# Kernel optimization log

Hardware: AMD Instinct MI355X
Metric: run time of the kernel (lower is better)

Reference implementation:

```python
import jax, jax.numpy as jnp
import numpy as np

B, S, D, H = 4, 2048, 1024, 16
W = D // H  # head width = 64


def setup_inputs() -> dict:
    key = jax.random.key(0)
    ks = jax.random.split(key, 7)
    sc = 0.02
    return {
        "x": jax.random.normal(ks[0], (B, S, D), dtype=jnp.float32),
        "mask": jnp.ones((B, S), dtype=jnp.int32),
        "Wq": jax.random.normal(ks[1], (D, D), dtype=jnp.float32) * sc,
        "bq": jax.random.normal(ks[2], (D,), dtype=jnp.float32) * sc,
        "Wk": jax.random.normal(ks[3], (D, D), dtype=jnp.float32) * sc,
        "bk": jax.random.normal(ks[4], (D,), dtype=jnp.float32) * sc,
        "Wv": jax.random.normal(ks[5], (D, D), dtype=jnp.float32) * sc,
        "bv": jax.random.normal(ks[6], (D,), dtype=jnp.float32) * sc,
    }


def reference(x, mask, Wq, bq, Wk, bk, Wv, bv):
    # Linear projections (torch Linear: y = x @ W.T + b)
    q = x @ Wq.T + bq  # (B,S,D)
    k = x @ Wk.T + bk
    v = x @ Wv.T + bv
    # split D -> (H, W) and move heads forward: (B,H,S,W)
    def split(t):
        return t.reshape(B, S, H, W).transpose(0, 2, 1, 3)
    q, k, v = split(q), split(k), split(v)
    scale = 1.0 / np.sqrt(W).astype(np.float32)
    scores = jnp.einsum("bhsw,bhtw->bhst", q, k) * scale  # (B,H,S,S)
    m = mask[:, None, None, :].astype(scores.dtype)  # (B,1,1,S)
    scores = scores - 10000.0 * (1.0 - m)
    probs = jax.nn.softmax(scores, axis=-1)  # dropout p=0.0 -> identity
    h = jnp.einsum("bhst,bhtw->bhsw", probs, v)  # (B,H,S,W)
    h = h.transpose(0, 2, 1, 3).reshape(B, S, D)  # merge heads
    return h
```

## Files before the change

kernel.cpp:

```cpp
#include <hip/hip_runtime.h>
#include <hip/hip_bf16.h>


#define NB 4
#define NS 2048
#define ND 1024
#define NH 16
#define NW 64

typedef __bf16 bf16;
typedef __bf16 bf16x2 __attribute__((ext_vector_type(2)));
typedef __bf16 bf16x4 __attribute__((ext_vector_type(4)));
typedef __bf16 bf16x8 __attribute__((ext_vector_type(8)));
typedef float f32x4 __attribute__((ext_vector_type(4)));
typedef float f32x16 __attribute__((ext_vector_type(16)));
typedef unsigned u32x4 __attribute__((ext_vector_type(4)));

__device__ __forceinline__ void gld_lds16(const void* g, void* l) {
  __builtin_amdgcn_global_load_lds(
      (const __attribute__((address_space(1))) void*)g,
      (__attribute__((address_space(3))) void*)l, 16, 0, 0);
}

__device__ __forceinline__ unsigned pack2(float lo, float hi) {
  bf16x2 t;
  t[0] = (bf16)lo;
  t[1] = (bf16)hi;
  return __builtin_bit_cast(unsigned, t);
}

__global__ void cast_f32_bf16(const float* __restrict__ src,
                              bf16* __restrict__ dst, int n) {
  int i = (blockIdx.x * blockDim.x + threadIdx.x) * 8;
  int stride = gridDim.x * blockDim.x * 8;
  for (; i < n; i += stride) {
    float4 a = *reinterpret_cast<const float4*>(src + i);
    float4 b = *reinterpret_cast<const float4*>(src + i + 4);
    bf16x8 o;
    o[0] = (bf16)a.x; o[1] = (bf16)a.y; o[2] = (bf16)a.z; o[3] = (bf16)a.w;
    o[4] = (bf16)b.x; o[5] = (bf16)b.y; o[6] = (bf16)b.z; o[7] = (bf16)b.w;
    *reinterpret_cast<bf16x8*>(dst + i) = o;
  }
}

__global__ void cast_weights(const float* __restrict__ a,
                             const float* __restrict__ b,
                             const float* __restrict__ c,
                             bf16* __restrict__ dst) {
  const int n = ND * ND;
  const int which = blockIdx.y;
  const float* src = (which == 0) ? a : ((which == 1) ? b : c);
  bf16* d = dst + (size_t)which * n;
  int i = (blockIdx.x * blockDim.x + threadIdx.x) * 8;
  float4 u = *reinterpret_cast<const float4*>(src + i);
  float4 v = *reinterpret_cast<const float4*>(src + i + 4);
  bf16x8 o;
  o[0] = (bf16)u.x; o[1] = (bf16)u.y; o[2] = (bf16)u.z; o[3] = (bf16)u.w;
  o[4] = (bf16)v.x; o[5] = (bf16)v.y; o[6] = (bf16)v.z; o[7] = (bf16)v.w;
  *reinterpret_cast<bf16x8*>(d + i) = o;
}

__global__ void mask_to_bf16(const int* __restrict__ mask,
                             bf16* __restrict__ mb, int n) {
  int i = blockIdx.x * blockDim.x + threadIdx.x;
  if (i < n) mb[i] = (bf16)(mask[i] ? 1.0f : 0.0f);
}

__global__ __launch_bounds__(256) void proj_kernel(
    const bf16* __restrict__ xb,
    const bf16* __restrict__ wq,
    const bf16* __restrict__ wk,
    const bf16* __restrict__ wv,
    const float* __restrict__ bq,
    const float* __restrict__ bk,
    const float* __restrict__ bv,
    const int* __restrict__ mask,
    bf16* __restrict__ qh,
    bf16* __restrict__ kh,
    bf16* __restrict__ vt) {
  const int mode = blockIdx.z;
  const bf16* wmat = (mode == 0) ? wq : ((mode == 1) ? wk : wv);
  const float* bias = (mode == 0) ? bq : ((mode == 1) ? bk : bv);

  __shared__ bf16 a_lds[128][64];
  __shared__ bf16 b_lds[128][64];

  const int tid = threadIdx.x;
  const int wave = tid >> 6;
  const int lane = tid & 63;
  const int wr = wave >> 1, wc = wave & 1;
  const int m0 = blockIdx.x * 128;
  const int n0 = blockIdx.y * 128;

  f32x4 acc[4][4] = {};

  const int srow = tid >> 3;
  const int scol = (tid & 7) * 8;
  const int sw_scol = scol ^ ((srow & 7) << 3);
  const int xr = (lane & 7) << 3;
  const int lr = lane & 15;
  const int kq = (lane >> 4) * 8;

  for (int k0 = 0; k0 < 1024; k0 += 64) {
#pragma unroll
    for (int c = 0; c < 4; ++c) {
      int row = srow + c * 32;
      gld_lds16(xb + (size_t)(m0 + row) * 1024 + k0 + sw_scol, &a_lds[row][scol]);
      gld_lds16(wmat + (size_t)(n0 + row) * 1024 + k0 + sw_scol, &b_lds[row][scol]);
    }
    __syncthreads();
#pragma unroll
    for (int kk = 0; kk < 64; kk += 32) {
      bf16x8 af[4], bfr[4];
      const int col = (kk + kq) ^ xr;
#pragma unroll
      for (int mf = 0; mf < 4; ++mf)
        af[mf] = *reinterpret_cast<const bf16x8*>(&a_lds[wr * 64 + mf * 16 + lr][col]);
#pragma unroll
      for (int nf = 0; nf < 4; ++nf)
        bfr[nf] = *reinterpret_cast<const bf16x8*>(&b_lds[wc * 64 + nf * 16 + lr][col]);
#pragma unroll
      for (int mf = 0; mf < 4; ++mf)
#pragma unroll
        for (int nf = 0; nf < 4; ++nf)
          acc[mf][nf] = __builtin_amdgcn_mfma_f32_16x16x32_bf16(af[mf], bfr[nf], acc[mf][nf], 0, 0, 0);
    }
    __syncthreads();
  }

  if (mode == 2) {
    float msk[4][4];
#pragma unroll
    for (int mf = 0; mf < 4; ++mf) {
      const int i0 = m0 + wr * 64 + mf * 16 + (lane >> 4) * 4;
      const int b = i0 >> 11, s = i0 & 2047;
      const int4 mm = *reinterpret_cast<const int4*>(mask + b * NS + s);
      msk[mf][0] = mm.x ? 1.f : 0.f;
      msk[mf][1] = mm.y ? 1.f : 0.f;
      msk[mf][2] = mm.z ? 1.f : 0.f;
      msk[mf][3] = mm.w ? 1.f : 0.f;
    }
#pragma unroll
    for (int nf = 0; nf < 4; ++nf) {
      const int j = n0 + wc * 64 + nf * 16 + lr;
      const float bj = bias[j];
      const int h = j >> 6, w = j & 63;
#pragma unroll
      for (int mf = 0; mf < 4; ++mf) {
        const int i0 = m0 + wr * 64 + mf * 16 + (lane >> 4) * 4;
        const int b = i0 >> 11, s = i0 & 2047;
        bf16x4 pk;
#pragma unroll
        for (int r = 0; r < 4; ++r)
          pk[r] = (bf16)((acc[mf][nf][r] + bj) * msk[mf][r]);
        *reinterpret_cast<bf16x4*>(&vt[(((size_t)(b * NH + h)) * NW + w) * NS + s]) = pk;
      }
    }
  } else {
    bf16* dst = (mode == 0) ? qh : kh;
#pragma unroll
    for (int nf = 0; nf < 4; ++nf) {
      const int j = n0 + wc * 64 + nf * 16 + lr;
      const float bj = bias[j];
      const int h = j >> 6, w = j & 63;
#pragma unroll
      for (int mf = 0; mf < 4; ++mf) {
        const int i0 = m0 + wr * 64 + mf * 16 + (lane >> 4) * 4;
        const int b = i0 >> 11, s = i0 & 2047;
#pragma unroll
        for (int r = 0; r < 4; ++r)
          dst[(((size_t)(b * NH + h)) * NS + s + r) * NW + w] = (bf16)(acc[mf][nf][r] + bj);
      }
    }
  }
}

__global__ __launch_bounds__(256, 4) void attn_kernel(
    const bf16* __restrict__ qh,
    const bf16* __restrict__ kh,
    const bf16* __restrict__ vt,
    const bf16* __restrict__ mb16,
    float* __restrict__ out) {
  __shared__ bf16 k_lds[2][64][64];
  __shared__ bf16 v_lds[2][64][64];

  const int tid = threadIdx.x;
  const int wave = tid >> 6;
  const int lane = tid & 63;
  const int lq = lane & 31;
  const int hi = lane >> 5;
  const int xr = (lq & 7) << 3;
  const int bh = blockIdx.y;
  const int b = bh >> 4;
  const int q0 = blockIdx.x * 128;
  const size_t headoff = (size_t)bh * NS * NW;

  bf16x8 qf[4];
  {
    const bf16* qp = qh + headoff + (size_t)(q0 + wave * 32 + lq) * NW + hi * 8;
#pragma unroll
    for (int m = 0; m < 4; ++m)
      qf[m] = *reinterpret_cast<const bf16x8*>(qp + m * 16);
  }

  f32x16 o0 = {}, o1 = {}, lt = {};
  const float SC2 = 0.18033688011112042f;
  const bf16* mp = mb16 + b * NS;

  const int srow = tid >> 3;
  const int scol = (tid & 7) * 8;
  const int sw_scol = scol ^ ((srow & 7) << 3);

#define STAGE(buf, kt)                                                          \
  {                                                                             \
    _Pragma("unroll") for (int c = 0; c < 2; ++c) {                             \
      const int row = srow + c * 32;                                            \
      gld_lds16(kh + headoff + (size_t)((kt) + row) * NW + sw_scol,             \
                &k_lds[buf][row][scol]);                                        \
      gld_lds16(vt + headoff + (size_t)row * NS + (kt) + sw_scol,               \
                &v_lds[buf][row][scol]);                                        \
    }                                                                           \
  }

#define QK_GROUP(G, PA0, PA1)                                                   \
  {                                                                             \
    f32x16 s = {};                                                              \
    __builtin_amdgcn_s_setprio(1);                                              \
    _Pragma("unroll") for (int m = 0; m < 4; ++m) {                             \
      bf16x8 kf = *reinterpret_cast<const bf16x8*>(                             \
          &k_lds[cur][(G) * 32 + lq][(m * 16 + hi * 8) ^ xr]);                  \
      s = __builtin_amdgcn_mfma_f32_32x32x16_bf16(kf, qf[m], s, 0, 0, 0);       \
    }                                                                           \
    __builtin_amdgcn_s_setprio(0);                                              \
    unsigned w[8];                                                              \
    _Pragma("unroll") for (int j = 0; j < 8; ++j)                               \
        w[j] = pack2(exp2f(s[2 * j] * SC2), exp2f(s[2 * j + 1] * SC2));         \
    asm("v_permlane32_swap_b32 %0, %1" : "+v"(w[0]), "+v"(w[2]));               \
    asm("v_permlane32_swap_b32 %0, %1" : "+v"(w[1]), "+v"(w[3]));               \
    asm("v_permlane32_swap_b32 %0, %1" : "+v"(w[4]), "+v"(w[6]));               \
    asm("v_permlane32_swap_b32 %0, %1" : "+v"(w[5]), "+v"(w[7]));               \
    u32x4 u0 = {w[0], w[1], w[2], w[3]};                                        \
    u32x4 u1 = {w[4], w[5], w[6], w[7]};                                        \
    PA0 = __builtin_bit_cast(bf16x8, u0);                                       \
    PA1 = __builtin_bit_cast(bf16x8, u1);                                       \
  }

#define PV_GROUP(G, PA0, PA1)                                                   \
  {                                                                             \
    const bf16* mpk = mp + kt + (G) * 32 + hi * 8;                              \
    bf16x8 mf0 = *reinterpret_cast<const bf16x8*>(mpk);                         \
    bf16x8 mf1 = *reinterpret_cast<const bf16x8*>(mpk + 16);                    \
    __builtin_amdgcn_s_setprio(1);                                              \
    lt = __builtin_amdgcn_mfma_f32_32x32x16_bf16(PA0, mf0, lt, 0, 0, 0);        \
    lt = __builtin_amdgcn_mfma_f32_32x32x16_bf16(PA1, mf1, lt, 0, 0, 0);        \
    bf16x8 v00 = *reinterpret_cast<const bf16x8*>(                              \
        &v_lds[cur][lq][((G) * 32 + hi * 8) ^ xr]);                             \
    o0 = __builtin_amdgcn_mfma_f32_32x32x16_bf16(PA0, v00, o0, 0, 0, 0);        \
    bf16x8 v01 = *reinterpret_cast<const bf16x8*>(                              \
        &v_lds[cur][lq][((G) * 32 + 16 + hi * 8) ^ xr]);                        \
    o0 = __builtin_amdgcn_mfma_f32_32x32x16_bf16(PA1, v01, o0, 0, 0, 0);        \
    bf16x8 v10 = *reinterpret_cast<const bf16x8*>(                              \
        &v_lds[cur][32 + lq][((G) * 32 + hi * 8) ^ xr]);                        \
    o1 = __builtin_amdgcn_mfma_f32_32x32x16_bf16(PA0, v10, o1, 0, 0, 0);        \
    bf16x8 v11 = *reinterpret_cast<const bf16x8*>(                              \
        &v_lds[cur][32 + lq][((G) * 32 + 16 + hi * 8) ^ xr]);                   \
    o1 = __builtin_amdgcn_mfma_f32_32x32x16_bf16(PA1, v11, o1, 0, 0, 0);        \
    __builtin_amdgcn_s_setprio(0);                                              \
  }

  STAGE(0, 0);
  __syncthreads();

  int cur = 0;
  for (int kt = 0; kt < NS; kt += 64) {
    if (kt + 64 < NS) STAGE(cur ^ 1, kt + 64);
    bf16x8 pa0, pa1, pa2, pa3;
    QK_GROUP(0, pa0, pa1);
    PV_GROUP(0, pa0, pa1);
    QK_GROUP(1, pa2, pa3);
    PV_GROUP(1, pa2, pa3);
    __syncthreads();
    cur ^= 1;
  }

  const int h = bh & 15;
  float* op = out + ((size_t)b * NS) * ND + h * NW;
#pragma unroll
  for (int r = 0; r < 16; ++r) {
    const int sq = q0 + wave * 32 + (r & 3) + 8 * (r >> 2) + 4 * hi;
    const float inv = 1.0f / lt[r];
    op[(size_t)sq * ND + lq] = o0[r] * inv;
    op[(size_t)sq * ND + 32 + lq] = o1[r] * inv;
  }
#undef STAGE
#undef QK_GROUP
#undef PV_GROUP
}

extern "C" void kernel_launch(void* const* d_in, const int* in_sizes, int n_in,
                              void* d_out, int out_size, void* d_ws, size_t ws_size,
                              hipStream_t stream) {
  const float* x = (const float*)d_in[0];
  const int* mask = (const int*)d_in[1];
  const float* Wq = (const float*)d_in[2];
  const float* bq = (const float*)d_in[3];
  const float* Wk = (const float*)d_in[4];
  const float* bk = (const float*)d_in[5];
  const float* Wv = (const float*)d_in[6];
  const float* bv = (const float*)d_in[7];
  float* out = (float*)d_out;

  char* ws = (char*)d_ws;
  bf16* wqb = (bf16*)(ws + (size_t)(0) * (1 << 20));
  bf16* wkb = (bf16*)(ws + (size_t)(2) * (1 << 20));
  bf16* wvb = (bf16*)(ws + (size_t)(4) * (1 << 20));
  bf16* qhb = (bf16*)(ws + (size_t)(6) * (1 << 20));
  bf16* khb = (bf16*)(ws + (size_t)(22) * (1 << 20));
  bf16* vtb = (bf16*)(ws + (size_t)(38) * (1 << 20));
  bf16* mb16 = (bf16*)(ws + (size_t)(54) * (1 << 20));
  bf16* xb = (bf16*)d_out;

  cast_f32_bf16<<<2048, 256, 0, stream>>>(x, xb, NB * NS * ND);
  cast_weights<<<dim3(512, 3), 256, 0, stream>>>(Wq, Wk, Wv, wqb);
  mask_to_bf16<<<32, 256, 0, stream>>>(mask, mb16, NB * NS);
  proj_kernel<<<dim3(64, 8, 3), 256, 0, stream>>>(xb, wqb, wkb, wvb, bq, bk, bv,
                                                  mask, qhb, khb, vtb);
  attn_kernel<<<dim3(NS / 128, NB * NH), 256, 0, stream>>>(qhb, khb, vtb, mb16, out);
}
```

Measured before the change: 301.3 us.

## Fold softmax scale into Q projection, vectorize Q/K stores, batch QK MFMAs, swizzle grid

The Q/K projection swaps MFMA operands so each lane holds four contiguous output columns. That allows vectorized bf16x4 stores and a vector bias load, and the softmax scale (log2e/sqrt(W)) is folded into Q at projection time. The attention kernel drops the per-element scale multiply before exp2, computes both 32-row QK tiles back to back before the exp/pack, and then runs all PV and row-sum MFMAs together. A 1D grid remaps block IDs across XCDs so blocks sharing a head's K/V land on the same die. Scaling Q before the bf16 rounding changes numerics slightly, and holding two score tiles live raises register pressure.

```diff
diff --git a/kernel.cpp b/kernel.cpp
--- a/kernel.cpp
+++ b/kernel.cpp
@@ -82,8 +82,8 @@
   const bf16* wmat = (mode == 0) ? wq : ((mode == 1) ? wk : wv);
   const float* bias = (mode == 0) ? bq : ((mode == 1) ? bk : bv);
 
-  __shared__ bf16 a_lds[128][64];
-  __shared__ bf16 b_lds[128][64];
+  __shared__ alignas(16) bf16 a_lds[128][64];
+  __shared__ alignas(16) bf16 b_lds[128][64];
 
   const int tid = threadIdx.x;
   const int wave = tid >> 6;
@@ -99,7 +99,8 @@
   const int sw_scol = scol ^ ((srow & 7) << 3);
   const int xr = (lane & 7) << 3;
   const int lr = lane & 15;
-  const int kq = (lane >> 4) * 8;
+  const int g = lane >> 4;
+  const int kq = g * 8;
 
   for (int k0 = 0; k0 < 1024; k0 += 64) {
 #pragma unroll
@@ -119,11 +120,19 @@
 #pragma unroll
       for (int nf = 0; nf < 4; ++nf)
         bfr[nf] = *reinterpret_cast<const bf16x8*>(&b_lds[wc * 64 + nf * 16 + lr][col]);
-#pragma unroll
-      for (int mf = 0; mf < 4; ++mf)
+      if (mode == 2) {
+#pragma unroll
+        for (int mf = 0; mf < 4; ++mf)
+#pragma unroll
+          for (int nf = 0; nf < 4; ++nf)
+            acc[mf][nf] = __builtin_amdgcn_mfma_f32_16x16x32_bf16(af[mf], bfr[nf], acc[mf][nf], 0, 0, 0);
+      } else {
 #pragma unroll
         for (int nf = 0; nf < 4; ++nf)
-          acc[mf][nf] = __builtin_amdgcn_mfma_f32_16x16x32_bf16(af[mf], bfr[nf], acc[mf][nf], 0, 0, 0);
+#pragma unroll
+          for (int mf = 0; mf < 4; ++mf)
+            acc[nf][mf] = __builtin_amdgcn_mfma_f32_16x16x32_bf16(bfr[nf], af[mf], acc[nf][mf], 0, 0, 0);
+      }
     }
     __syncthreads();
   }
@@ -132,7 +141,7 @@
     float msk[4][4];
 #pragma unroll
     for (int mf = 0; mf < 4; ++mf) {
-      const int i0 = m0 + wr * 64 + mf * 16 + (lane >> 4) * 4;
+      const int i0 = m0 + wr * 64 + mf * 16 + g * 4;
       const int b = i0 >> 11, s = i0 & 2047;
       const int4 mm = *reinterpret_cast<const int4*>(mask + b * NS + s);
       msk[mf][0] = mm.x ? 1.f : 0.f;
@@ -147,7 +156,7 @@
       const int h = j >> 6, w = j & 63;
 #pragma unroll
       for (int mf = 0; mf < 4; ++mf) {
-        const int i0 = m0 + wr * 64 + mf * 16 + (lane >> 4) * 4;
+        const int i0 = m0 + wr * 64 + mf * 16 + g * 4;
         const int b = i0 >> 11, s = i0 & 2047;
         bf16x4 pk;
 #pragma unroll
@@ -158,18 +167,21 @@
     }
   } else {
     bf16* dst = (mode == 0) ? qh : kh;
+    const float scl = (mode == 0) ? 0.18033688011112042f : 1.0f;
 #pragma unroll
     for (int nf = 0; nf < 4; ++nf) {
-      const int j = n0 + wc * 64 + nf * 16 + lr;
-      const float bj = bias[j];
-      const int h = j >> 6, w = j & 63;
+      const int j0 = n0 + wc * 64 + nf * 16 + g * 4;
+      const f32x4 bj = *reinterpret_cast<const f32x4*>(&bias[j0]);
+      const int h = j0 >> 6, w0 = j0 & 63;
 #pragma unroll
       for (int mf = 0; mf < 4; ++mf) {
-        const int i0 = m0 + wr * 64 + mf * 16 + (lane >> 4) * 4;
-        const int b = i0 >> 11, s = i0 & 2047;
+        const int i = m0 + wr * 64 + mf * 16 + lr;
+        const int b = i >> 11, s = i & 2047;
+        bf16x4 pk;
 #pragma unroll
         for (int r = 0; r < 4; ++r)
-          dst[(((size_t)(b * NH + h)) * NS + s + r) * NW + w] = (bf16)(acc[mf][nf][r] + bj);
+          pk[r] = (bf16)((acc[nf][mf][r] + bj[r]) * scl);
+        *reinterpret_cast<bf16x4*>(&dst[(((size_t)(b * NH + h)) * NS + s) * NW + w0]) = pk;
       }
     }
   }
@@ -181,8 +193,8 @@
     const bf16* __restrict__ vt,
     const bf16* __restrict__ mb16,
     float* __restrict__ out) {
-  __shared__ bf16 k_lds[2][64][64];
-  __shared__ bf16 v_lds[2][64][64];
+  __shared__ alignas(16) bf16 k_lds[2][64][64];
+  __shared__ alignas(16) bf16 v_lds[2][64][64];
 
   const int tid = threadIdx.x;
   const int wave = tid >> 6;
@@ -190,9 +202,12 @@
   const int lq = lane & 31;
   const int hi = lane >> 5;
   const int xr = (lq & 7) << 3;
-  const int bh = blockIdx.y;
+
+  const int p = blockIdx.x;
+  const int w_id = (p & 7) * 128 + (p >> 3);
+  const int bh = w_id >> 4;
   const int b = bh >> 4;
-  const int q0 = blockIdx.x * 128;
+  const int q0 = (w_id & 15) * 128;
   const size_t headoff = (size_t)bh * NS * NW;
 
   bf16x8 qf[4];
@@ -204,7 +219,6 @@
   }
 
   f32x16 o0 = {}, o1 = {}, lt = {};
-  const float SC2 = 0.18033688011112042f;
   const bf16* mp = mb16 + b * NS;
 
   const int srow = tid >> 3;
@@ -222,50 +236,19 @@
     }                                                                           \
   }
 
-#define QK_GROUP(G, PA0, PA1)                                                   \
+#define EXPPACK(S, PA0, PA1)                                                    \
   {                                                                             \
-    f32x16 s = {};                                                              \
-    __builtin_amdgcn_s_setprio(1);                                              \
-    _Pragma("unroll") for (int m = 0; m < 4; ++m) {                             \
-      bf16x8 kf = *reinterpret_cast<const bf16x8*>(                             \
-          &k_lds[cur][(G) * 32 + lq][(m * 16 + hi * 8) ^ xr]);                  \
-      s = __builtin_amdgcn_mfma_f32_32x32x16_bf16(kf, qf[m], s, 0, 0, 0);       \
-    }                                                                           \
-    __builtin_amdgcn_s_setprio(0);                                              \
-    unsigned w[8];                                                              \
+    unsigned w_[8];                                                             \
     _Pragma("unroll") for (int j = 0; j < 8; ++j)                               \
-        w[j] = pack2(exp2f(s[2 * j] * SC2), exp2f(s[2 * j + 1] * SC2));         \
-    asm("v_permlane32_swap_b32 %0, %1" : "+v"(w[0]), "+v"(w[2]));               \
-    asm("v_permlane32_swap_b32 %0, %1" : "+v"(w[1]), "+v"(w[3]));               \
-    asm("v_permlane32_swap_b32 %0, %1" : "+v"(w[4]), "+v"(w[6]));               \
-    asm("v_permlane32_swap_b32 %0, %1" : "+v"(w[5]), "+v"(w[7]));               \
-    u32x4 u0 = {w[0], w[1], w[2], w[3]};                                        \
-    u32x4 u1 = {w[4], w[5], w[6], w[7]};                                        \
+        w_[j] = pack2(exp2f(S[2 * j]), exp2f(S[2 * j + 1]));                    \
+    asm("v_permlane32_swap_b32 %0, %1" : "+v"(w_[0]), "+v"(w_[2]));             \
+    asm("v_permlane32_swap_b32 %0, %1" : "+v"(w_[1]), "+v"(w_[3]));             \
+    asm("v_permlane32_swap_b32 %0, %1" : "+v"(w_[4]), "+v"(w_[6]));             \
+    asm("v_permlane32_swap_b32 %0, %1" : "+v"(w_[5]), "+v"(w_[7]));             \
+    u32x4 u0 = {w_[0], w_[1], w_[2], w_[3]};                                    \
+    u32x4 u1 = {w_[4], w_[5], w_[6], w_[7]};                                    \
     PA0 = __builtin_bit_cast(bf16x8, u0);                                       \
     PA1 = __builtin_bit_cast(bf16x8, u1);                                       \
-  }
-
-#define PV_GROUP(G, PA0, PA1)                                                   \
-  {                                                                             \
-    const bf16* mpk = mp + kt + (G) * 32 + hi * 8;                              \
-    bf16x8 mf0 = *reinterpret_cast<const bf16x8*>(mpk);                         \
-    bf16x8 mf1 = *reinterpret_cast<const bf16x8*>(mpk + 16);                    \
-    __builtin_amdgcn_s_setprio(1);                                              \
-    lt = __builtin_amdgcn_mfma_f32_32x32x16_bf16(PA0, mf0, lt, 0, 0, 0);        \
-    lt = __builtin_amdgcn_mfma_f32_32x32x16_bf16(PA1, mf1, lt, 0, 0, 0);        \
-    bf16x8 v00 = *reinterpret_cast<const bf16x8*>(                              \
-        &v_lds[cur][lq][((G) * 32 + hi * 8) ^ xr]);                             \
-    o0 = __builtin_amdgcn_mfma_f32_32x32x16_bf16(PA0, v00, o0, 0, 0, 0);        \
-    bf16x8 v01 = *reinterpret_cast<const bf16x8*>(                              \
-        &v_lds[cur][lq][((G) * 32 + 16 + hi * 8) ^ xr]);                        \
-    o0 = __builtin_amdgcn_mfma_f32_32x32x16_bf16(PA1, v01, o0, 0, 0, 0);        \
-    bf16x8 v10 = *reinterpret_cast<const bf16x8*>(                              \
-        &v_lds[cur][32 + lq][((G) * 32 + hi * 8) ^ xr]);                        \
-    o1 = __builtin_amdgcn_mfma_f32_32x32x16_bf16(PA0, v10, o1, 0, 0, 0);        \
-    bf16x8 v11 = *reinterpret_cast<const bf16x8*>(                              \
-        &v_lds[cur][32 + lq][((G) * 32 + 16 + hi * 8) ^ xr]);                   \
-    o1 = __builtin_amdgcn_mfma_f32_32x32x16_bf16(PA1, v11, o1, 0, 0, 0);        \
-    __builtin_amdgcn_s_setprio(0);                                              \
   }
 
   STAGE(0, 0);
@@ -274,11 +257,51 @@
   int cur = 0;
   for (int kt = 0; kt < NS; kt += 64) {
     if (kt + 64 < NS) STAGE(cur ^ 1, kt + 64);
+
+    f32x16 s0 = {}, s1 = {};
+    __builtin_amdgcn_s_setprio(1);
+#pragma unroll
+    for (int m = 0; m < 4; ++m) {
+      const int col = (m * 16 + hi * 8) ^ xr;
+      bf16x8 kf0 = *reinterpret_cast<const bf16x8*>(&k_lds[cur][lq][col]);
+      s0 = __builtin_amdgcn_mfma_f32_32x32x16_bf16(kf0, qf[m], s0, 0, 0, 0);
+      bf16x8 kf1 = *reinterpret_cast<const bf16x8*>(&k_lds[cur][32 + lq][col]);
+      s1 = __builtin_amdgcn_mfma_f32_32x32x16_bf16(kf1, qf[m], s1, 0, 0, 0);
+    }
+    __builtin_amdgcn_s_setprio(0);
+
     bf16x8 pa0, pa1, pa2, pa3;
-    QK_GROUP(0, pa0, pa1);
-    PV_GROUP(0, pa0, pa1);
-    QK_GROUP(1, pa2, pa3);
-    PV_GROUP(1, pa2, pa3);
+    EXPPACK(s0, pa0, pa1);
+    EXPPACK(s1, pa2, pa3);
+
+    const bf16* mpk = mp + kt + hi * 8;
+    bf16x8 mf00 = *reinterpret_cast<const bf16x8*>(mpk);
+    bf16x8 mf01 = *reinterpret_cast<const bf16x8*>(mpk + 16);
+    bf16x8 mf10 = *reinterpret_cast<const bf16x8*>(mpk + 32);
+    bf16x8 mf11 = *reinterpret_cast<const bf16x8*>(mpk + 48);
+
+    __builtin_amdgcn_s_setprio(1);
+    lt = __builtin_amdgcn_mfma_f32_32x32x16_bf16(pa0, mf00, lt, 0, 0, 0);
+    lt = __builtin_amdgcn_mfma_f32_32x32x16_bf16(pa1, mf01, lt, 0, 0, 0);
+    lt = __builtin_amdgcn_mfma_f32_32x32x16_bf16(pa2, mf10, lt, 0, 0, 0);
+    lt = __builtin_amdgcn_mfma_f32_32x32x16_bf16(pa3, mf11, lt, 0, 0, 0);
+#pragma unroll
+    for (int G = 0; G < 2; ++G) {
+      const bf16x8 a0 = G ? pa2 : pa0;
+      const bf16x8 a1 = G ? pa3 : pa1;
+      const int c0 = (G * 32 + hi * 8) ^ xr;
+      const int c1 = (G * 32 + 16 + hi * 8) ^ xr;
+      bf16x8 v00 = *reinterpret_cast<const bf16x8*>(&v_lds[cur][lq][c0]);
+      o0 = __builtin_amdgcn_mfma_f32_32x32x16_bf16(a0, v00, o0, 0, 0, 0);
+      bf16x8 v01 = *reinterpret_cast<const bf16x8*>(&v_lds[cur][lq][c1]);
+      o0 = __builtin_amdgcn_mfma_f32_32x32x16_bf16(a1, v01, o0, 0, 0, 0);
+      bf16x8 v10 = *reinterpret_cast<const bf16x8*>(&v_lds[cur][32 + lq][c0]);
+      o1 = __builtin_amdgcn_mfma_f32_32x32x16_bf16(a0, v10, o1, 0, 0, 0);
+      bf16x8 v11 = *reinterpret_cast<const bf16x8*>(&v_lds[cur][32 + lq][c1]);
+      o1 = __builtin_amdgcn_mfma_f32_32x32x16_bf16(a1, v11, o1, 0, 0, 0);
+    }
+    __builtin_amdgcn_s_setprio(0);
+
     __syncthreads();
     cur ^= 1;
   }
@@ -293,8 +316,7 @@
     op[(size_t)sq * ND + 32 + lq] = o1[r] * inv;
   }
 #undef STAGE
-#undef QK_GROUP
-#undef PV_GROUP
+#undef EXPPACK
 }
 
 extern "C" void kernel_launch(void* const* d_in, const int* in_sizes, int n_in,
@@ -325,5 +347,5 @@
   mask_to_bf16<<<32, 256, 0, stream>>>(mask, mb16, NB * NS);
   proj_kernel<<<dim3(64, 8, 3), 256, 0, stream>>>(xb, wqb, wkb, wvb, bq, bk, bv,
                                                   mask, qhb, khb, vtb);
-  attn_kernel<<<dim3(NS / 128, NB * NH), 256, 0, stream>>>(qhb, khb, vtb, mb16, out);
-}
+  attn_kernel<<<1024, 256, 0, stream>>>(qhb, khb, vtb, mb16, out);
+}
```

After: 310.3 us. 1.03x slower.
